# Kernel optimization log

Hardware: AMD Instinct MI355X
Metric: run time of the kernel (lower is better)

Reference implementation:

```python
import jax, jax.numpy as jnp
import numpy as np

WS = 8        # window_size
SHIFT = 4     # shift_size
NH = 6        # num_heads
EPS = 1e-5


def _rel_pos_index(ws):
    coords = np.stack(np.meshgrid(np.arange(ws), np.arange(ws), indexing='ij'))  # [2,ws,ws]
    cf = coords.reshape(2, -1)                      # [2, ws*ws]
    rel = cf[:, :, None] - cf[:, None, :]           # [2, N, N]
    rel = rel.transpose(1, 2, 0)                    # [N, N, 2]
    rel[:, :, 0] += ws - 1
    rel[:, :, 1] += ws - 1
    rel[:, :, 0] *= 2 * ws - 1
    return rel.sum(-1)                              # [N, N] int


def _attn_mask(H, W, ws, shift):
    img = np.zeros((H, W), dtype=np.float32)
    slices = (slice(0, -ws), slice(-ws, -shift), slice(-shift, None))
    cnt = 0
    for hs in slices:
        for wsl in slices:
            img[hs, wsl] = cnt
            cnt += 1
    mw = img.reshape(H // ws, ws, W // ws, ws).transpose(0, 2, 1, 3).reshape(-1, ws * ws)
    diff = mw[:, None, :] - mw[:, :, None]          # [nW, N, N]
    return np.where(diff != 0, -100.0, 0.0).astype(np.float32)


def _layernorm(x, g, b):
    mu = x.mean(-1, keepdims=True)
    var = ((x - mu) ** 2).mean(-1, keepdims=True)
    return (x - mu) * jax.lax.rsqrt(var + EPS) * g + b


def setup_inputs() -> dict:
    key = jax.random.key(0)
    ks = jax.random.split(key, 8)
    C, HID = 192, 768
    return {
        'x': jax.random.normal(ks[0], (8, 128, 128, C), jnp.float32),
        'g1': jnp.ones((C,), jnp.float32),
        'b1': jnp.zeros((C,), jnp.float32),
        'qkv_w': jax.random.normal(ks[1], (3 * C, C), jnp.float32) * 0.02,
        'qkv_b': jnp.zeros((3 * C,), jnp.float32),
        'rpb_table': jax.random.normal(ks[2], ((2 * WS - 1) ** 2, NH), jnp.float32) * 0.02,
        'proj_w': jax.random.normal(ks[3], (C, C), jnp.float32) * 0.02,
        'proj_b': jnp.zeros((C,), jnp.float32),
        'g2': jnp.ones((C,), jnp.float32),
        'b2': jnp.zeros((C,), jnp.float32),
        'fc1_w': jax.random.normal(ks[4], (HID, C), jnp.float32) * 0.02,
        'fc1_b': jnp.zeros((HID,), jnp.float32),
        'fc2_w': jax.random.normal(ks[5], (C, HID), jnp.float32) * 0.02,
        'fc2_b': jnp.zeros((C,), jnp.float32),
    }


def reference(x, g1, b1, qkv_w, qkv_b, rpb_table, proj_w, proj_b, g2, b2,
              fc1_w, fc1_b, fc2_w, fc2_b):
    B, H, W, C = x.shape
    N = WS * WS
    hd = C // NH
    scale = hd ** -0.5

    rpi = jnp.asarray(_rel_pos_index(WS))                 # [N,N] static
    mask = jnp.asarray(_attn_mask(H, W, WS, SHIFT))       # [nW,N,N] static
    nW = mask.shape[0]

    shortcut = x.reshape(B, H * W, C)
    xn = _layernorm(shortcut, g1, b1).reshape(B, H, W, C)

    # cyclic shift
    xs = jnp.roll(xn, shift=(-SHIFT, -SHIFT), axis=(1, 2))

    # window partition -> [B*nW, N, C]
    win = xs.reshape(B, H // WS, WS, W // WS, WS, C).transpose(0, 1, 3, 2, 4, 5)
    win = win.reshape(-1, N, C)
    B_ = win.shape[0]

    # qkv
    qkv = jnp.einsum('bnc,oc->bno', win, qkv_w) + qkv_b   # [B_,N,3C]
    qkv = qkv.reshape(B_, N, 3, NH, hd).transpose(2, 0, 3, 1, 4)  # [3,B_,NH,N,hd]
    q, k, v = qkv[0] * scale, qkv[1], qkv[2]

    attn = jnp.einsum('bhnd,bhmd->bhnm', q, k)            # [B_,NH,N,N]
    bias = rpb_table[rpi.reshape(-1)].reshape(N, N, NH).transpose(2, 0, 1)
    attn = attn + bias[None]
    attn = attn.reshape(B, nW, NH, N, N) + mask[None, :, None]
    attn = jax.nn.softmax(attn.reshape(B_, NH, N, N), axis=-1)

    out = jnp.einsum('bhnm,bhmd->bhnd', attn, v)          # [B_,NH,N,hd]
    out = out.transpose(0, 2, 1, 3).reshape(B_, N, C)
    out = jnp.einsum('bnc,oc->bno', out, proj_w) + proj_b

    # window reverse -> [B,H,W,C]
    out = out.reshape(B, H // WS, W // WS, WS, WS, C).transpose(0, 1, 3, 2, 4, 5)
    out = out.reshape(B, H, W, C)
    out = jnp.roll(out, shift=(SHIFT, SHIFT), axis=(1, 2)).reshape(B, H * W, C)

    x1 = shortcut + out
    h = _layernorm(x1, g2, b2)
    h = jnp.einsum('bnc,hc->bnh', h, fc1_w) + fc1_b
    h = jax.nn.gelu(h, approximate=False)
    h = jnp.einsum('bnh,ch->bnc', h, fc2_w) + fc2_b
    x2 = x1 + h
    return x2.reshape(B, H, W, C)
```

## Files before the change

### kernel.cpp

```cpp
#include <hip/hip_runtime.h>
#include <hip/hip_bf16.h>

typedef __attribute__((ext_vector_type(8))) short s16x8;
typedef __attribute__((ext_vector_type(4))) float f32x4;

__device__ __forceinline__ unsigned short f2bf(float f){
    __hip_bfloat16 h = __float2bfloat16(f);
    return *reinterpret_cast<unsigned short*>(&h);
}

__device__ __forceinline__ int flab(int g){ return (g < 120) ? 0 : ((g < 124) ? 1 : 2); }

__device__ __forceinline__ void async16(const void* g, void* l){
    __builtin_amdgcn_global_load_lds(
        (const __attribute__((address_space(1))) unsigned int*)g,
        (__attribute__((address_space(3))) unsigned int*)l, 16, 0, 0);
}

__global__ __launch_bounds__(256) void wconv_all(
    const float* __restrict__ w0, const float* __restrict__ w1,
    const float* __restrict__ w2, const float* __restrict__ w3,
    unsigned short* __restrict__ o0, unsigned short* __restrict__ o1,
    unsigned short* __restrict__ o2, unsigned short* __restrict__ o3)
{
    int i = blockIdx.x*256 + threadIdx.x;
    if (i < 110592) o0[i] = f2bf(w0[i]);
    if (i < 36864)  o1[i] = f2bf(w1[i]);
    if (i < 147456) {
        int o = i/192, k = i - o*192;
        int oc = o/192, r = o - oc*192, ks = k>>5, c = k&31;
        o2[((oc*6 + ks)*192 + r)*32 + c] = f2bf(w2[i]);
    }
    if (i < 147456) {
        int o = i/768, k = i - o*768;
        int q = o/48, r = o - q*48, ks = k>>5, c = k&31;
        o3[((q*24 + ks)*48 + r)*32 + c] = f2bf(w3[i]);
    }
}

__global__ __launch_bounds__(256) void lnqkv_kernel(
    const float* __restrict__ x, const float* __restrict__ g1, const float* __restrict__ b1,
    const unsigned short* __restrict__ wq, const float* __restrict__ qkvb,
    unsigned short* __restrict__ qo, unsigned short* __restrict__ ko,
    unsigned short* __restrict__ vo)
{
    __shared__ __attribute__((aligned(16))) unsigned short win[64*200];
    __shared__ __attribute__((aligned(16))) unsigned short Bs[64*200];
    const int b_ = blockIdx.x;
    const int bb = b_>>8, wi = b_&255, wh = wi>>4, ww = wi&15;
    const int tid = threadIdx.x;
    const int wv = tid>>6, lane = tid&63, lrow = lane&15, quad = lane>>4;

    {
        const int n = tid>>2, q4 = tid&3;
        const int r = n>>3, c = n&7;
        const int hh = (wh*8 + r + 4)&127, wp = (ww*8 + c + 4)&127;
        const float* px = x + (((size_t)bb*128+hh)*128+wp)*192 + q4*48;
        float v[48];
        #pragma unroll
        for (int m=0;m<12;++m) *(float4*)(v+m*4) = *(const float4*)(px+m*4);
        float s = 0.f;
        #pragma unroll
        for (int k=0;k<48;++k) s += v[k];
        s += __shfl_xor(s,1); s += __shfl_xor(s,2);
        float mu = s*(1.0f/192.0f);
        float qv = 0.f;
        #pragma unroll
        for (int k=0;k<48;++k){ float d=v[k]-mu; qv += d*d; }
        qv += __shfl_xor(qv,1); qv += __shfl_xor(qv,2);
        float rstd = rsqrtf(qv*(1.0f/192.0f) + 1e-5f);
        const float* pg = g1 + q4*48;
        const float* pb = b1 + q4*48;
        unsigned short* pw = win + n*200 + q4*48;
        #pragma unroll
        for (int k=0;k<48;++k) pw[k] = f2bf((v[k]-mu)*rstd*pg[k] + pb[k]);
    }
    __syncthreads();

    s16x8 af[6];
    #pragma unroll
    for (int kc=0;kc<6;++kc)
        af[kc] = *(const s16x8*)(win + (wv*16+lrow)*200 + kc*32 + quad*8);

    for (int ot=0; ot<9; ++ot) {
        const int o0 = ot*64;
        __syncthreads();
        #pragma unroll
        for (int t=0;t<6;++t) {
            int cid = tid + t*256;
            *(int4*)(Bs + (cid/24)*200 + (cid%24)*8) =
                *(const int4*)(wq + (size_t)o0*192 + cid*8);
        }
        __syncthreads();
        f32x4 acc[4];
        #pragma unroll
        for (int j=0;j<4;++j) acc[j] = (f32x4){0.f,0.f,0.f,0.f};
        #pragma unroll
        for (int kc=0;kc<6;++kc)
            #pragma unroll
            for (int j=0;j<4;++j) {
                s16x8 bf = *(const s16x8*)(Bs + (j*16+lrow)*200 + kc*32 + quad*8);
                acc[j] = __builtin_amdgcn_mfma_f32_16x16x32_bf16(af[kc], bf, acc[j], 0, 0, 0);
            }
        __syncthreads();
        unsigned short* T = Bs;
        const int part = ot/3;
        float bv[4];
        #pragma unroll
        for (int j=0;j<4;++j) bv[j] = qkvb[o0 + j*16 + lrow];

        if (part < 2) {
            const float scale = (part==0) ? 0.17677669529663687f : 1.0f;
            #pragma unroll
            for (int j=0;j<4;++j)
                #pragma unroll
                for (int rg=0;rg<4;++rg) {
                    int n2 = wv*16 + quad*4 + rg;
                    T[n2*72 + j*16 + lrow] = f2bf((acc[j][rg]+bv[j])*scale);
                }
            __syncthreads();
            unsigned short* dst = (part==0) ? qo : ko;
            #pragma unroll
            for (int t=0;t<2;++t) {
                int c = tid + t*256;
                int n2 = c>>3, blk = c&7;
                int o_in = o0 + blk*8 - part*192;
                int head = o_in>>5, d = o_in&31;
                *(int4*)(dst + (((size_t)b_*6+head)*64 + n2)*32 + d) =
                    *(const int4*)(T + n2*72 + blk*8);
            }
        } else {
            #pragma unroll
            for (int j=0;j<4;++j)
                #pragma unroll
                for (int rg=0;rg<4;++rg) {
                    int n2 = wv*16 + quad*4 + rg;
                    T[(j*16+lrow)*72 + n2] = f2bf(acc[j][rg]+bv[j]);
                }
            __syncthreads();
            #pragma unroll
            for (int t=0;t<2;++t) {
                int c = tid + t*256;
                int ol = c>>3, nb = (c&7)*8;
                int o_in = o0 + ol - 384;
                int head = o_in>>5, d = o_in&31;
                *(int4*)(vo + (((size_t)b_*6+head)*32 + d)*64 + nb) =
                    *(const int4*)(T + ol*72 + nb);
            }
        }
    }
}

__global__ __launch_bounds__(384) void attn_kernel(
    const unsigned short* __restrict__ q, const unsigned short* __restrict__ k,
    const unsigned short* __restrict__ vT, const float* __restrict__ rpb,
    unsigned short* __restrict__ ao)
{
    __shared__ float rpb_s[1350];
    __shared__ __attribute__((aligned(16))) unsigned short p_lds[6*4608];
    const int b_ = blockIdx.x;
    const int h = threadIdx.x >> 6;
    const int lane = threadIdx.x & 63, lrow = lane & 15, quad = lane >> 4;
    for (int i = threadIdx.x; i < 1350; i += 384) rpb_s[i] = rpb[i];
    __syncthreads();

    const size_t hb = ((size_t)b_*6 + h)*2048;
    const unsigned short* qb = q  + hb;
    const unsigned short* kb = k  + hb;
    const unsigned short* vb = vT + hb;

    s16x8 qf[4], kf[4];
    #pragma unroll
    for (int i = 0; i < 4; ++i) qf[i] = *(const s16x8*)(qb + (i*16+lrow)*32 + quad*8);
    #pragma unroll
    for (int j = 0; j < 4; ++j) kf[j] = *(const s16x8*)(kb + (j*16+lrow)*32 + quad*8);

    const f32x4 zz = {0.f,0.f,0.f,0.f};
    f32x4 s[4][4];
    #pragma unroll
    for (int i = 0; i < 4; ++i)
        #pragma unroll
        for (int j = 0; j < 4; ++j)
            s[i][j] = __builtin_amdgcn_mfma_f32_16x16x32_bf16(qf[i], kf[j], zz, 0, 0, 0);

    const int wi = b_ & 255, wh = wi >> 4, ww = wi & 15;
    int labm[4];
    #pragma unroll
    for (int j = 0; j < 4; ++j) {
        int m = j*16 + lrow;
        labm[j] = flab(wh*8 + (m >> 3))*3 + flab(ww*8 + (m & 7));
    }
    unsigned short* pl = p_lds + h*4608;
    #pragma unroll
    for (int i = 0; i < 4; ++i) {
        #pragma unroll
        for (int rg = 0; rg < 4; ++rg) {
            int n = i*16 + quad*4 + rg;
            int rn = n >> 3, cn = n & 7;
            int labn = flab(wh*8 + rn)*3 + flab(ww*8 + cn);
            float vals[4];
            float vmax = -1e30f;
            #pragma unroll
            for (int j = 0; j < 4; ++j) {
                int m = j*16 + lrow;
                int idx = ((rn - (m >> 3) + 7)*15 + (cn - (m & 7) + 7))*6 + h;
                float val = s[i][j][rg] + rpb_s[idx];
                if (labn != labm[j]) val -= 100.f;
                vals[j] = val;
                vmax = fmaxf(vmax, val);
            }
            #pragma unroll
            for (int o = 1; o < 16; o <<= 1) vmax = fmaxf(vmax, __shfl_xor(vmax, o));
            float sum = 0.f;
            #pragma unroll
            for (int j = 0; j < 4; ++j) { vals[j] = __expf(vals[j] - vmax); sum += vals[j]; }
            #pragma unroll
            for (int o = 1; o < 16; o <<= 1) sum += __shfl_xor(sum, o);
            float inv = 1.f / sum;
            #pragma unroll
            for (int j = 0; j < 4; ++j) pl[n*72 + j*16 + lrow] = f2bf(vals[j]*inv);
        }
    }
    __syncthreads();

    f32x4 oacc[4][2];
    #pragma unroll
    for (int i = 0; i < 4; ++i) { oacc[i][0] = zz; oacc[i][1] = zz; }
    #pragma unroll
    for (int kc = 0; kc < 2; ++kc) {
        s16x8 vf[2];
        #pragma unroll
        for (int jd = 0; jd < 2; ++jd)
            vf[jd] = *(const s16x8*)(vb + (jd*16+lrow)*64 + kc*32 + quad*8);
        #pragma unroll
        for (int i = 0; i < 4; ++i) {
            s16x8 pf = *(const s16x8*)(pl + (i*16+lrow)*72 + kc*32 + quad*8);
            #pragma unroll
            for (int jd = 0; jd < 2; ++jd)
                oacc[i][jd] = __builtin_amdgcn_mfma_f32_16x16x32_bf16(pf, vf[jd], oacc[i][jd], 0, 0, 0);
        }
    }
    unsigned short* ob = ao + (size_t)b_*12288 + h*32;
    #pragma unroll
    for (int i = 0; i < 4; ++i)
        #pragma unroll
        for (int jd = 0; jd < 2; ++jd)
            #pragma unroll
            for (int rg = 0; rg < 4; ++rg) {
                int n = i*16 + quad*4 + rg;
                ob[(size_t)n*192 + jd*16 + lrow] = f2bf(oacc[i][jd][rg]);
            }
}

__device__ __forceinline__ void mm64x192(
    const unsigned short* __restrict__ A, const unsigned short* __restrict__ W,
    size_t m0, unsigned short* As, unsigned short* Bs, f32x4 (&acc)[12])
{
    const int tid = threadIdx.x, wv = tid>>6, lane = tid&63;
    const int lrow = lane&15, quad = lane>>4;
    const int grow = lane>>2;
    const int gcb  = (lane&3) ^ ((lane>>3)&3);
    #pragma unroll
    for (int j=0;j<12;++j) acc[j] = (f32x4){0.f,0.f,0.f,0.f};

    const unsigned short* Ab = A + (m0 + grow)*192 + gcb*8;
    const unsigned short* Wb = W + (size_t)grow*192 + gcb*8;

    auto issue = [&](int k0, unsigned short* Ad, unsigned short* Bd) {
        async16(Ab + (size_t)(wv*16)*192 + k0,     Ad + wv*512);
        async16(Wb + (size_t)(wv*16)*192 + k0,     Bd + wv*512);
        async16(Wb + (size_t)((wv+4)*16)*192 + k0, Bd + (wv+4)*512);
        async16(Wb + (size_t)((wv+8)*16)*192 + k0, Bd + (wv+8)*512);
    };
    issue(0, As, Bs);
    int cur = 0;
    for (int k0=0; k0<192; k0+=32) {
        __syncthreads();
        if (k0+32 < 192) issue(k0+32, As + (cur^1)*2048, Bs + (cur^1)*6144);
        const unsigned short* Ac = As + cur*2048;
        const unsigned short* Bc = Bs + cur*6144;
        const int rs = (quad ^ ((lrow>>1)&3)) << 3;
        s16x8 af = *(const s16x8*)(Ac + (wv*16+lrow)*32 + rs);
        #pragma unroll
        for (int j=0;j<12;++j) {
            s16x8 bf = *(const s16x8*)(Bc + (j*16+lrow)*32 + rs);
            acc[j] = __builtin_amdgcn_mfma_f32_16x16x32_bf16(af, bf, acc[j], 0, 0, 0);
        }
        cur ^= 1;
    }
}

__global__ __launch_bounds__(256) void projln_kernel(
    const unsigned short* __restrict__ A, const unsigned short* __restrict__ W,
    const float* __restrict__ pbias, const float* __restrict__ x,
    const float* __restrict__ g2, const float* __restrict__ b2,
    float* __restrict__ x1, unsigned short* __restrict__ xln2b)
{
    __shared__ __attribute__((aligned(16))) char smem[32768];
    unsigned short* As = (unsigned short*)smem;
    unsigned short* Bs = (unsigned short*)(smem + 8192);
    const int b_ = blockIdx.x;
    const int tid = threadIdx.x, wv = tid>>6, lane = tid&63;
    const int lrow = lane&15, quad = lane>>4;
    const size_t m0 = (size_t)b_*64;

    f32x4 acc[12];
    mm64x192(A, W, m0, As, Bs, acc);
    __syncthreads();

    const int bb = b_>>8, wi = b_&255, wh = wi>>4, ww = wi&15;
    float bv[12], gv[12], b2v[12];
    #pragma unroll
    for (int j=0;j<12;++j) {
        bv[j]  = pbias[j*16+lrow];
        gv[j]  = g2[j*16+lrow];
        b2v[j] = b2[j*16+lrow];
    }
    unsigned short* T = (unsigned short*)smem;
    #pragma unroll
    for (int rg=0;rg<4;++rg) {
        int n2 = wv*16 + quad*4 + rg;
        int r = n2>>3, c = n2&7;
        int hh = (wh*8+r+4)&127, wp = (ww*8+c+4)&127;
        size_t tok = ((size_t)bb*128+hh)*128 + wp;
        float xv[12];
        float s = 0.f;
        #pragma unroll
        for (int j=0;j<12;++j) {
            float t = acc[j][rg] + bv[j] + x[tok*192 + j*16 + lrow];
            xv[j] = t; s += t;
        }
        #pragma unroll
        for (int o=1;o<16;o<<=1) s += __shfl_xor(s, o);
        float mu = s*(1.0f/192.0f);
        float qv = 0.f;
        #pragma unroll
        for (int j=0;j<12;++j){ float d = xv[j]-mu; qv += d*d; }
        #pragma unroll
        for (int o=1;o<16;o<<=1) qv += __shfl_xor(qv, o);
        float rstd = rsqrtf(qv*(1.0f/192.0f) + 1e-5f);
        #pragma unroll
        for (int j=0;j<12;++j) {
            x1[tok*192 + j*16 + lrow] = xv[j];
            T[n2*200 + j*16 + lrow] = f2bf((xv[j]-mu)*rstd*gv[j] + b2v[j]);
        }
    }
    __syncthreads();
    #pragma unroll
    for (int t=0;t<6;++t) {
        int cid = tid + t*256;
        int n2 = cid/24, blk = cid%24;
        int r = n2>>3, c = n2&7;
        int hh = (wh*8+r+4)&127, wp = (ww*8+c+4)&127;
        size_t tok = ((size_t)bb*128+hh)*128 + wp;
        int row = (int)(tok & 127);
        int ks = blk>>2, kb = blk&3;
        int sw = (kb ^ ((row>>1)&3)) << 3;
        *(int4*)(xln2b + (tok>>7)*24576 + ks*4096 + row*32 + sw) =
            *(const int4*)(T + n2*200 + blk*8);
    }
}

__global__ __launch_bounds__(512, 4) void mlp_kernel(
    const unsigned short* __restrict__ Ablk,
    const unsigned short* __restrict__ W1b,
    const float* __restrict__ fc1b,
    const unsigned short* __restrict__ W2b,
    const float* __restrict__ fc2b,
    const float* __restrict__ x1, float* __restrict__ out)
{
    __shared__ __attribute__((aligned(16))) unsigned short Ald[6*2048];
    __shared__ __attribute__((aligned(16))) unsigned short Hld[6*2048];
    const int b_ = blockIdx.x;
    const int mt = b_>>1, half = b_&1;
    const int tid = threadIdx.x, wv = tid>>6, lane = tid&63;
    const int lrow = lane&15, quad = lane>>4;
    const int wr = wv>>2, wc = wv&3;
    const int r0 = wr*32, c0 = wc*48;
    const int rs = (quad ^ ((lrow>>1)&3)) << 3;

    {
        const unsigned short* src = Ablk + (size_t)mt*24576 + half*2048 + lane*8;
        #pragma unroll
        for (int r=0;r<3;++r) {
            int c = r*8 + wv;
            async16(src + (c>>2)*4096 + (c&3)*512, Ald + c*512);
        }
    }

    float bv1[4][3];
    #pragma unroll
    for (int oc=0;oc<4;++oc)
        #pragma unroll
        for (int j=0;j<3;++j) bv1[oc][j] = fc1b[oc*192 + c0 + j*16 + lrow];

    f32x4 a2[2][3];
    #pragma unroll
    for (int i=0;i<2;++i)
        #pragma unroll
        for (int j=0;j<3;++j) a2[i][j] = (f32x4){0.f,0.f,0.f,0.f};

    const unsigned short* w1base = W1b + (size_t)c0*32 + quad*8;
    s16x8 b1c[3];
    #pragma unroll
    for (int j=0;j<3;++j) b1c[j] = *(const s16x8*)(w1base + (j*16 + lrow)*32);

    __syncthreads();

    for (int oc=0; oc<4; ++oc) {
        const unsigned short* w1p = w1base + (size_t)(oc*6)*6144;
        f32x4 a1[2][3];
        #pragma unroll
        for (int i=0;i<2;++i)
            #pragma unroll
            for (int j=0;j<3;++j) a1[i][j] = (f32x4){0.f,0.f,0.f,0.f};
        #pragma unroll
        for (int ks=0;ks<6;++ks) {
            s16x8 b1n[3];
            if (ks < 5) {
                #pragma unroll
                for (int j=0;j<3;++j)
                    b1n[j] = *(const s16x8*)(w1p + (size_t)(ks+1)*6144 + (j*16 + lrow)*32);
            }
            s16x8 af[2];
            #pragma unroll
            for (int i=0;i<2;++i)
                af[i] = *(const s16x8*)(Ald + ks*2048 + (r0 + i*16 + lrow)*32 + rs);
            #pragma unroll
            for (int i=0;i<2;++i)
                #pragma unroll
                for (int j=0;j<3;++j)
                    a1[i][j] = __builtin_amdgcn_mfma_f32_16x16x32_bf16(af[i], b1c[j], a1[i][j], 0, 0, 0);
            if (ks < 5) { b1c[0]=b1n[0]; b1c[1]=b1n[1]; b1c[2]=b1n[2]; }
        }

        const unsigned short* w2p = W2b + (size_t)(wc*24 + oc*6)*1536 + quad*8;
        s16x8 b2c[3];
        #pragma unroll
        for (int j=0;j<3;++j) b2c[j] = *(const s16x8*)(w2p + (j*16 + lrow)*32);
        if (oc < 3) {
            #pragma unroll
            for (int j=0;j<3;++j)
                b1c[j] = *(const s16x8*)(w1base + (size_t)((oc+1)*6)*6144 + (j*16 + lrow)*32);
        }

        if (oc) __syncthreads();

        #pragma unroll
        for (int i=0;i<2;++i)
            #pragma unroll
            for (int j=0;j<3;++j)
                #pragma unroll
                for (int rg=0;rg<4;++rg) {
                    int row = r0 + i*16 + quad*4 + rg;
                    int o = c0 + j*16 + lrow;
                    float v = a1[i][j][rg] + bv1[oc][j];
                    float v2 = v*v;
                    float z = v*(1.5957691216057308f + 0.07135481627f*v2);
                    float r = v * __builtin_amdgcn_rcpf(1.f + __expf(-z));
                    int ksh = o>>5, c5 = o&31;
                    Hld[ksh*2048 + row*32 + (((c5>>3) ^ ((row>>1)&3))<<3) + (c5&7)] = f2bf(r);
                }
        __syncthreads();

        #pragma unroll
        for (int ksl=0;ksl<6;++ksl) {
            s16x8 b2n[3];
            if (ksl < 5) {
                #pragma unroll
                for (int j=0;j<3;++j)
                    b2n[j] = *(const s16x8*)(w2p + (size_t)(ksl+1)*1536 + (j*16 + lrow)*32);
            }
            s16x8 af2[2];
            #pragma unroll
            for (int i=0;i<2;++i)
                af2[i] = *(const s16x8*)(Hld + ksl*2048 + (r0 + i*16 + lrow)*32 + rs);
            #pragma unroll
            for (int i=0;i<2;++i)
                #pragma unroll
                for (int j=0;j<3;++j)
                    a2[i][j] = __builtin_amdgcn_mfma_f32_16x16x32_bf16(af2[i], b2c[j], a2[i][j], 0, 0, 0);
            if (ksl < 5) { b2c[0]=b2n[0]; b2c[1]=b2n[1]; b2c[2]=b2n[2]; }
        }
    }

    {
        float bv2[3];
        #pragma unroll
        for (int j=0;j<3;++j) bv2[j] = fc2b[c0 + j*16 + lrow];
        #pragma unroll
        for (int i=0;i<2;++i)
            #pragma unroll
            for (int j=0;j<3;++j)
                #pragma unroll
                for (int rg=0;rg<4;++rg) {
                    size_t grow = (size_t)mt*128 + half*64 + r0 + i*16 + quad*4 + rg;
                    size_t ad = grow*192 + c0 + j*16 + lrow;
                    out[ad] = a2[i][j][rg] + bv2[j] + x1[ad];
                }
    }
}

extern "C" void kernel_launch(void* const* d_in, const int* in_sizes, int n_in,
                              void* d_out, int out_size, void* d_ws, size_t ws_size,
                              hipStream_t stream)
{
    const float* x      = (const float*)d_in[0];
    const float* g1     = (const float*)d_in[1];
    const float* b1     = (const float*)d_in[2];
    const float* qkv_w  = (const float*)d_in[3];
    const float* qkv_b  = (const float*)d_in[4];
    const float* rpb    = (const float*)d_in[5];
    const float* proj_w = (const float*)d_in[6];
    const float* proj_b = (const float*)d_in[7];
    const float* g2     = (const float*)d_in[8];
    const float* b2     = (const float*)d_in[9];
    const float* fc1_w  = (const float*)d_in[10];
    const float* fc1_b  = (const float*)d_in[11];
    const float* fc2_w  = (const float*)d_in[12];
    const float* fc2_b  = (const float*)d_in[13];
    float* out = (float*)d_out;
    char* ws = (char*)d_ws;

    if (ws_size < 353206272ULL) return;

    unsigned short* qbuf  = (unsigned short*)(ws + 0);
    unsigned short* kbuf  = (unsigned short*)(ws + 50331648);
    unsigned short* vbuf  = (unsigned short*)(ws + 100663296);
    unsigned short* attnO = (unsigned short*)(ws + 150994944);
    float*          x1    = (float*)        (ws + 201326592);
    unsigned short* xln2  = (unsigned short*)(ws + 301989888);
    unsigned short* wq    = (unsigned short*)(ws + 352321536);
    unsigned short* wp    = (unsigned short*)(ws + 352321536 + 221184);
    unsigned short* w1b   = (unsigned short*)(ws + 352321536 + 221184 + 73728);
    unsigned short* w2b   = (unsigned short*)(ws + 352321536 + 221184 + 73728 + 294912);

    wconv_all<<<576, 256, 0, stream>>>(qkv_w, proj_w, fc1_w, fc2_w, wq, wp, w1b, w2b);
    lnqkv_kernel<<<2048, 256, 0, stream>>>(x, g1, b1, wq, qkv_b, qbuf, kbuf, vbuf);
    attn_kernel<<<2048, 384, 0, stream>>>(qbuf, kbuf, vbuf, rpb, attnO);
    projln_kernel<<<2048, 256, 0, stream>>>(attnO, wp, proj_b, x, g2, b2, x1, xln2);
    mlp_kernel<<<2048, 512, 0, stream>>>(xln2, w1b, fc1_b, w2b, fc2_b, x1, out);
}
```

Before: 544.8 us.

## Warp-specialize MLP kernel into fc1 and fc2 wave groups with double-buffered hidden tile

```diff
diff --git a/kernel.cpp b/kernel.cpp
--- a/kernel.cpp
+++ b/kernel.cpp
@@ -370,13 +370,14 @@
     const float* __restrict__ x1, float* __restrict__ out)
 {
     __shared__ __attribute__((aligned(16))) unsigned short Ald[6*2048];
-    __shared__ __attribute__((aligned(16))) unsigned short Hld[6*2048];
+    __shared__ __attribute__((aligned(16))) unsigned short Hld[2*6*2048];
     const int b_ = blockIdx.x;
     const int mt = b_>>1, half = b_&1;
     const int tid = threadIdx.x, wv = tid>>6, lane = tid&63;
     const int lrow = lane&15, quad = lane>>4;
-    const int wr = wv>>2, wc = wv&3;
-    const int r0 = wr*32, c0 = wc*48;
+    const bool fc1w = (wv < 4);
+    const int w4 = wv & 3;
+    const int c0 = w4*48;
     const int rs = (quad ^ ((lrow>>1)&3)) << 3;
 
     {
@@ -388,115 +389,122 @@
         }
     }
 
-    float bv1[4][3];
-    #pragma unroll
-    for (int oc=0;oc<4;++oc)
-        #pragma unroll
-        for (int j=0;j<3;++j) bv1[oc][j] = fc1b[oc*192 + c0 + j*16 + lrow];
-
-    f32x4 a2[2][3];
-    #pragma unroll
-    for (int i=0;i<2;++i)
-        #pragma unroll
-        for (int j=0;j<3;++j) a2[i][j] = (f32x4){0.f,0.f,0.f,0.f};
+    f32x4 acc[4][3];
+    #pragma unroll
+    for (int i=0;i<4;++i)
+        #pragma unroll
+        for (int j=0;j<3;++j) acc[i][j] = (f32x4){0.f,0.f,0.f,0.f};
 
     const unsigned short* w1base = W1b + (size_t)c0*32 + quad*8;
-    s16x8 b1c[3];
-    #pragma unroll
-    for (int j=0;j<3;++j) b1c[j] = *(const s16x8*)(w1base + (j*16 + lrow)*32);
+    const unsigned short* w2base = W2b + (size_t)(w4*24)*1536 + quad*8;
+    s16x8 bc[3];
+    #pragma unroll
+    for (int j=0;j<3;++j)
+        bc[j] = fc1w ? *(const s16x8*)(w1base + (j*16+lrow)*32)
+                     : *(const s16x8*)(w2base + (j*16+lrow)*32);
 
     __syncthreads();
 
-    for (int oc=0; oc<4; ++oc) {
-        const unsigned short* w1p = w1base + (size_t)(oc*6)*6144;
-        f32x4 a1[2][3];
-        #pragma unroll
-        for (int i=0;i<2;++i)
-            #pragma unroll
-            for (int j=0;j<3;++j) a1[i][j] = (f32x4){0.f,0.f,0.f,0.f};
-        #pragma unroll
-        for (int ks=0;ks<6;++ks) {
-            s16x8 b1n[3];
-            if (ks < 5) {
-                #pragma unroll
-                for (int j=0;j<3;++j)
-                    b1n[j] = *(const s16x8*)(w1p + (size_t)(ks+1)*6144 + (j*16 + lrow)*32);
-            }
-            s16x8 af[2];
-            #pragma unroll
-            for (int i=0;i<2;++i)
-                af[i] = *(const s16x8*)(Ald + ks*2048 + (r0 + i*16 + lrow)*32 + rs);
-            #pragma unroll
-            for (int i=0;i<2;++i)
-                #pragma unroll
-                for (int j=0;j<3;++j)
-                    a1[i][j] = __builtin_amdgcn_mfma_f32_16x16x32_bf16(af[i], b1c[j], a1[i][j], 0, 0, 0);
-            if (ks < 5) { b1c[0]=b1n[0]; b1c[1]=b1n[1]; b1c[2]=b1n[2]; }
-        }
-
-        const unsigned short* w2p = W2b + (size_t)(wc*24 + oc*6)*1536 + quad*8;
-        s16x8 b2c[3];
-        #pragma unroll
-        for (int j=0;j<3;++j) b2c[j] = *(const s16x8*)(w2p + (j*16 + lrow)*32);
-        if (oc < 3) {
+    for (int ph = 0; ph < 5; ++ph) {
+        if (fc1w) {
+            if (ph < 4) {
+                const int oc = ph;
+                float bv[3];
+                #pragma unroll
+                for (int j=0;j<3;++j) bv[j] = fc1b[oc*192 + c0 + j*16 + lrow];
+                #pragma unroll
+                for (int i=0;i<4;++i)
+                    #pragma unroll
+                    for (int j=0;j<3;++j) acc[i][j] = (f32x4){0.f,0.f,0.f,0.f};
+                const unsigned short* w1p = w1base + (size_t)(oc*6)*6144;
+                #pragma unroll
+                for (int ks=0;ks<6;++ks) {
+                    s16x8 bn[3];
+                    if (ks < 5) {
+                        #pragma unroll
+                        for (int j=0;j<3;++j)
+                            bn[j] = *(const s16x8*)(w1p + (size_t)(ks+1)*6144 + (j*16 + lrow)*32);
+                    }
+                    s16x8 af[4];
+                    #pragma unroll
+                    for (int i=0;i<4;++i)
+                        af[i] = *(const s16x8*)(Ald + ks*2048 + (i*16 + lrow)*32 + rs);
+                    #pragma unroll
+                    for (int i=0;i<4;++i)
+                        #pragma unroll
+                        for (int j=0;j<3;++j)
+                            acc[i][j] = __builtin_amdgcn_mfma_f32_16x16x32_bf16(af[i], bc[j], acc[i][j], 0, 0, 0);
+                    if (ks < 5) { bc[0]=bn[0]; bc[1]=bn[1]; bc[2]=bn[2]; }
+                }
+                if (oc < 3) {
+                    #pragma unroll
+                    for (int j=0;j<3;++j)
+                        bc[j] = *(const s16x8*)(w1base + (size_t)((oc+1)*6)*6144 + (j*16 + lrow)*32);
+                }
+                unsigned short* Hb = Hld + (ph&1)*12288;
+                #pragma unroll
+                for (int i=0;i<4;++i)
+                    #pragma unroll
+                    for (int j=0;j<3;++j)
+                        #pragma unroll
+                        for (int rg=0;rg<4;++rg) {
+                            int row = i*16 + quad*4 + rg;
+                            int o = c0 + j*16 + lrow;
+                            float v = acc[i][j][rg] + bv[j];
+                            float v2 = v*v;
+                            float z = v*(1.5957691216057308f + 0.07135481627f*v2);
+                            float r = v * __builtin_amdgcn_rcpf(1.f + __expf(-z));
+                            int ksh = o>>5, c5 = o&31;
+                            Hb[ksh*2048 + row*32 + (((c5>>3) ^ ((row>>1)&3))<<3) + (c5&7)] = f2bf(r);
+                        }
+            }
+        } else {
+            if (ph >= 1) {
+                const int oc = ph - 1;
+                const unsigned short* Hb = Hld + (oc&1)*12288;
+                const unsigned short* w2p = w2base + (size_t)(oc*6)*1536;
+                #pragma unroll
+                for (int ksl=0;ksl<6;++ksl) {
+                    s16x8 bn[3];
+                    if (ksl < 5) {
+                        #pragma unroll
+                        for (int j=0;j<3;++j)
+                            bn[j] = *(const s16x8*)(w2p + (size_t)(ksl+1)*1536 + (j*16 + lrow)*32);
+                    }
+                    s16x8 af[4];
+                    #pragma unroll
+                    for (int i=0;i<4;++i)
+                        af[i] = *(const s16x8*)(Hb + ksl*2048 + (i*16 + lrow)*32 + rs);
+                    #pragma unroll
+                    for (int i=0;i<4;++i)
+                        #pragma unroll
+                        for (int j=0;j<3;++j)
+                            acc[i][j] = __builtin_amdgcn_mfma_f32_16x16x32_bf16(af[i], bc[j], acc[i][j], 0, 0, 0);
+                    if (ksl < 5) { bc[0]=bn[0]; bc[1]=bn[1]; bc[2]=bn[2]; }
+                }
+                if (oc < 3) {
+                    #pragma unroll
+                    for (int j=0;j<3;++j)
+                        bc[j] = *(const s16x8*)(w2base + (size_t)((oc+1)*6)*1536 + (j*16 + lrow)*32);
+                }
+            }
+        }
+        __syncthreads();
+    }
+
+    if (!fc1w) {
+        float bv2[3];
+        #pragma unroll
+        for (int j=0;j<3;++j) bv2[j] = fc2b[c0 + j*16 + lrow];
+        #pragma unroll
+        for (int i=0;i<4;++i)
             #pragma unroll
             for (int j=0;j<3;++j)
-                b1c[j] = *(const s16x8*)(w1base + (size_t)((oc+1)*6)*6144 + (j*16 + lrow)*32);
-        }
-
-        if (oc) __syncthreads();
-
-        #pragma unroll
-        for (int i=0;i<2;++i)
-            #pragma unroll
-            for (int j=0;j<3;++j)
                 #pragma unroll
                 for (int rg=0;rg<4;++rg) {
-                    int row = r0 + i*16 + quad*4 + rg;
-                    int o = c0 + j*16 + lrow;
-                    float v = a1[i][j][rg] + bv1[oc][j];
-                    float v2 = v*v;
-                    float z = v*(1.5957691216057308f + 0.07135481627f*v2);
-                    float r = v * __builtin_amdgcn_rcpf(1.f + __expf(-z));
-                    int ksh = o>>5, c5 = o&31;
-                    Hld[ksh*2048 + row*32 + (((c5>>3) ^ ((row>>1)&3))<<3) + (c5&7)] = f2bf(r);
-                }
-        __syncthreads();
-
-        #pragma unroll
-        for (int ksl=0;ksl<6;++ksl) {
-            s16x8 b2n[3];
-            if (ksl < 5) {
-                #pragma unroll
-                for (int j=0;j<3;++j)
-                    b2n[j] = *(const s16x8*)(w2p + (size_t)(ksl+1)*1536 + (j*16 + lrow)*32);
-            }
-            s16x8 af2[2];
-            #pragma unroll
-            for (int i=0;i<2;++i)
-                af2[i] = *(const s16x8*)(Hld + ksl*2048 + (r0 + i*16 + lrow)*32 + rs);
-            #pragma unroll
-            for (int i=0;i<2;++i)
-                #pragma unroll
-                for (int j=0;j<3;++j)
-                    a2[i][j] = __builtin_amdgcn_mfma_f32_16x16x32_bf16(af2[i], b2c[j], a2[i][j], 0, 0, 0);
-            if (ksl < 5) { b2c[0]=b2n[0]; b2c[1]=b2n[1]; b2c[2]=b2n[2]; }
-        }
-    }
-
-    {
-        float bv2[3];
-        #pragma unroll
-        for (int j=0;j<3;++j) bv2[j] = fc2b[c0 + j*16 + lrow];
-        #pragma unroll
-        for (int i=0;i<2;++i)
-            #pragma unroll
-            for (int j=0;j<3;++j)
-                #pragma unroll
-                for (int rg=0;rg<4;++rg) {
-                    size_t grow = (size_t)mt*128 + half*64 + r0 + i*16 + quad*4 + rg;
+                    size_t grow = (size_t)mt*128 + half*64 + i*16 + quad*4 + rg;
                     size_t ad = grow*192 + c0 + j*16 + lrow;
-                    out[ad] = a2[i][j][rg] + bv2[j] + x1[ad];
+                    out[ad] = acc[i][j][rg] + bv2[j] + x1[ad];
                 }
     }
 }
```

New measurement: 664.6 us. 22.0% more time.
